# Optimization experiments

Measured on AMD Instinct MI355X. Metric: run time of the kernel, lower is better.

The kernel has to match this reference:

```python
import jax, jax.numpy as jnp
import numpy as np

HEADS = 4
DIM_HEAD = 32
SCALE = DIM_HEAD ** -0.5


def setup_inputs() -> dict:
    key = jax.random.key(0)
    k1, k2, k3 = jax.random.split(key, 3)
    dim = 128
    hidden = HEADS * DIM_HEAD  # 128
    x = jax.random.normal(k1, (4, dim, 64, 64), dtype=jnp.float32)
    w_qkv = jax.random.normal(k2, (3 * hidden, dim), dtype=jnp.float32) * (dim ** -0.5)
    w_out = jax.random.normal(k3, (dim, hidden), dtype=jnp.float32) * (hidden ** -0.5)
    b_out = jnp.zeros((dim,), dtype=jnp.float32)
    return {"x": x, "w_qkv": w_qkv, "w_out": w_out, "b_out": b_out}


def reference(x, w_qkv, w_out, b_out):
    b, c, h, w = x.shape
    n = h * w
    # 1x1 conv == channel matmul per pixel
    qkv = jnp.einsum('oc,bchw->bohw', w_qkv, x)  # [b, 3*hidden, h, w]
    q, k, v = jnp.split(qkv, 3, axis=1)
    # b (heads d) x y -> b heads d (x y)
    def to_heads(t):
        return t.reshape(b, HEADS, DIM_HEAD, n)
    q = to_heads(q) * SCALE
    k = to_heads(k)
    v = to_heads(v)
    sim = jnp.einsum('bhdi,bhdj->bhij', q, k)          # [b, heads, n, n]
    attn = jax.nn.softmax(sim, axis=-1)
    out = jnp.einsum('bhij,bhdj->bhid', attn, v)        # [b, heads, n, d]
    # b h (x y) d -> b (h d) x y
    out = out.transpose(0, 1, 3, 2).reshape(b, HEADS * DIM_HEAD, h, w)
    out = jnp.einsum('oc,bchw->bohw', w_out, out) + b_out[None, :, None, None]
    return out
```

## Files before the change

kernel.cpp:

```cpp
#include <hip/hip_runtime.h>
#include <math.h>

#define NHEAD 4
#define DHEAD 32
#define NPIX  4096
#define CIN   128

typedef __bf16 bf16_t;
typedef __bf16 bf16x8 __attribute__((ext_vector_type(8)));
typedef __bf16 bf16x4 __attribute__((ext_vector_type(4)));
typedef float  f32x4  __attribute__((ext_vector_type(4)));

constexpr float QSCALE = 0.17677669529663687f * 1.4426950408889634f;

__global__ void __launch_bounds__(256) prep_swz(
    const float* __restrict__ wqkv, const float* __restrict__ wout,
    ushort* __restrict__ wq_s, ushort* __restrict__ wo_s) {
  const int gid = blockIdx.x * 256 + threadIdx.x;
  const int lane = gid & 63, n = lane & 15, quad = (lane >> 4) & 3;
  if (gid < 6144) {
    const int ot = gid >> 8, k = (gid >> 6) & 3;
    const float sc = (ot < 8) ? QSCALE : 1.f;
    const float* src = wqkv + (size_t)(ot * 16 + n) * CIN + k * 32 + quad * 8;
    bf16x8 o;
#pragma unroll
    for (int e = 0; e < 8; ++e) o[e] = (bf16_t)(src[e] * sc);
    *(bf16x8*)(wq_s + (size_t)gid * 8) = o;
  } else {
    const int oid = gid - 6144;
    const int ot = oid >> 8, k = (oid >> 6) & 3;
    const float* src = wout + (size_t)(ot * 16 + n) * CIN + k * 32 + quad * 8;
    bf16x8 o;
#pragma unroll
    for (int e = 0; e < 8; ++e) o[e] = (bf16_t)src[e];
    *(bf16x8*)(wo_s + (size_t)oid * 8) = o;
  }
}

__global__ void __launch_bounds__(256) qkv_mfma(
    const float* __restrict__ x, const ushort* __restrict__ wq_s,
    ushort* __restrict__ qb, ushort* __restrict__ kb, ushort* __restrict__ vT) {
  __shared__ ushort Xls[32 * 136];
  const int blk = blockIdx.x, tid = threadIdx.x;
  const int wave = tid >> 6, lane = tid & 63;
  const int n = lane & 15, quad = lane >> 4;
  const int bb = blk >> 7;
  const int p0 = (blk & 127) * 32;

  {
    const int pc = tid & 7, c0 = (tid >> 3) * 4;
    const float* xp = x + ((size_t)bb * CIN + c0) * NPIX + p0 + pc * 4;
    float4 r0 = *(const float4*)xp;
    float4 r1 = *(const float4*)(xp + NPIX);
    float4 r2 = *(const float4*)(xp + 2 * NPIX);
    float4 r3 = *(const float4*)(xp + 3 * NPIX);
    bf16x4 w0 = {(bf16_t)r0.x, (bf16_t)r1.x, (bf16_t)r2.x, (bf16_t)r3.x};
    bf16x4 w1 = {(bf16_t)r0.y, (bf16_t)r1.y, (bf16_t)r2.y, (bf16_t)r3.y};
    bf16x4 w2 = {(bf16_t)r0.z, (bf16_t)r1.z, (bf16_t)r2.z, (bf16_t)r3.z};
    bf16x4 w3 = {(bf16_t)r0.w, (bf16_t)r1.w, (bf16_t)r2.w, (bf16_t)r3.w};
    *(bf16x4*)&Xls[(pc * 4 + 0) * 136 + c0] = w0;
    *(bf16x4*)&Xls[(pc * 4 + 1) * 136 + c0] = w1;
    *(bf16x4*)&Xls[(pc * 4 + 2) * 136 + c0] = w2;
    *(bf16x4*)&Xls[(pc * 4 + 3) * 136 + c0] = w3;
  }
  __syncthreads();

  bf16x8 xf[2][4];
#pragma unroll
  for (int nt = 0; nt < 2; ++nt)
#pragma unroll
    for (int k = 0; k < 4; ++k)
      xf[nt][k] = *(const bf16x8*)&Xls[(nt * 16 + n) * 136 + k * 32 + quad * 8];

#pragma unroll
  for (int mt = 0; mt < 6; ++mt) {
    const int ot = wave * 6 + mt;
    const int type = ot >> 3;
    const int wt = ot & 7, head = wt >> 1, d0 = (wt & 1) * 16;
    const int bh = bb * NHEAD + head;
    bf16x8 wf4[4];
#pragma unroll
    for (int k = 0; k < 4; ++k)
      wf4[k] = *(const bf16x8*)(wq_s + (size_t)((ot * 4 + k) * 64 + lane) * 8);
    f32x4 acc[2] = {{0.f, 0.f, 0.f, 0.f}, {0.f, 0.f, 0.f, 0.f}};
    if (type < 2) {
#pragma unroll
      for (int k = 0; k < 4; ++k)
#pragma unroll
        for (int nt = 0; nt < 2; ++nt)
          acc[nt] = __builtin_amdgcn_mfma_f32_16x16x32_bf16(wf4[k], xf[nt][k], acc[nt], 0, 0, 0);
      ushort* dst = (type == 0) ? qb : kb;
#pragma unroll
      for (int nt = 0; nt < 2; ++nt) {
        bf16x4 o = {(bf16_t)acc[nt][0], (bf16_t)acc[nt][1],
                    (bf16_t)acc[nt][2], (bf16_t)acc[nt][3]};
        *(bf16x4*)(dst + ((size_t)bh * NPIX + p0 + nt * 16 + n) * DHEAD + d0 + quad * 4) = o;
      }
    } else {
#pragma unroll
      for (int k = 0; k < 4; ++k)
#pragma unroll
        for (int nt = 0; nt < 2; ++nt)
          acc[nt] = __builtin_amdgcn_mfma_f32_16x16x32_bf16(xf[nt][k], wf4[k], acc[nt], 0, 0, 0);
#pragma unroll
      for (int nt = 0; nt < 2; ++nt) {
        bf16x4 o = {(bf16_t)acc[nt][0], (bf16_t)acc[nt][1],
                    (bf16_t)acc[nt][2], (bf16_t)acc[nt][3]};
        *(bf16x4*)(vT + ((size_t)bh * DHEAD + d0 + n) * NPIX + p0 + nt * 16 + quad * 4) = o;
      }
    }
  }
}

__device__ __forceinline__ void ft_load(const ushort* kb0, const ushort* vb0,
                                        int t, bf16x8* kf, bf16x8* vf) {
#pragma unroll
  for (int p = 0; p < 2; ++p) {
#pragma unroll
    for (int s = 0; s < 2; ++s)
      kf[p * 2 + s] = *(const bf16x8*)(kb0 + (size_t)(t * 64 + p * 32 + s * 4) * DHEAD);
#pragma unroll
    for (int dp = 0; dp < 2; ++dp)
      vf[p * 2 + dp] = *(const bf16x8*)(vb0 + (size_t)dp * 16 * NPIX + t * 64 + p * 32);
  }
}

__device__ __forceinline__ void ft_compute(const bf16x8* qf, const bf16x8* kf,
                                           const bf16x8* vf, const bf16x8 ones,
                                           f32x4 O[8][2], f32x4* Ol) {
  const f32x4 zero = {0.f, 0.f, 0.f, 0.f};
#pragma unroll
  for (int p = 0; p < 2; ++p) {
#pragma unroll
    for (int rp = 0; rp < 8; ++rp) {
      f32x4 sa = __builtin_amdgcn_mfma_f32_16x16x32_bf16(kf[p * 2 + 0], qf[rp], zero, 0, 0, 0);
      f32x4 sb = __builtin_amdgcn_mfma_f32_16x16x32_bf16(kf[p * 2 + 1], qf[rp], zero, 0, 0, 0);
      bf16x8 pf;
#pragma unroll
      for (int r = 0; r < 4; ++r) {
        pf[r]     = (bf16_t)__builtin_amdgcn_exp2f(sa[r]);
        pf[r + 4] = (bf16_t)__builtin_amdgcn_exp2f(sb[r]);
      }
      O[rp][0] = __builtin_amdgcn_mfma_f32_16x16x32_bf16(pf, vf[p * 2 + 0], O[rp][0], 0, 0, 0);
      O[rp][1] = __builtin_amdgcn_mfma_f32_16x16x32_bf16(pf, vf[p * 2 + 1], O[rp][1], 0, 0, 0);
      Ol[rp]   = __builtin_amdgcn_mfma_f32_16x16x32_bf16(pf, ones, Ol[rp], 0, 0, 0);
    }
  }
}

__global__ void __launch_bounds__(256, 2) flash_mfma(
    const ushort* __restrict__ qb, const ushort* __restrict__ kbuf,
    const ushort* __restrict__ vTb, float* __restrict__ part) {
  const int tid = threadIdx.x, wave = tid >> 6, lane = tid & 63;
  const int n = lane & 15, quad = lane >> 4;
  const int js = blockIdx.y, bh = blockIdx.z;
  const int qrel = blockIdx.x * 512 + wave * 128;

  const ushort* kg = kbuf + (size_t)bh * NPIX * DHEAD;
  const ushort* vg = vTb + (size_t)bh * DHEAD * NPIX;

  bf16x8 qf[8];
#pragma unroll
  for (int rp = 0; rp < 8; ++rp)
    qf[rp] = *(const bf16x8*)(qb +
        ((size_t)bh * NPIX + qrel + rp * 16 + n) * DHEAD + quad * 8);

  f32x4 O[8][2], Ol[8];
#pragma unroll
  for (int rp = 0; rp < 8; ++rp) {
    O[rp][0] = (f32x4){0.f, 0.f, 0.f, 0.f};
    O[rp][1] = (f32x4){0.f, 0.f, 0.f, 0.f};
    Ol[rp]   = (f32x4){0.f, 0.f, 0.f, 0.f};
  }
  const bf16_t one = (bf16_t)1.0f;
  const bf16x8 ones = {one, one, one, one, one, one, one, one};

  const int pk = ((n >> 2) << 3) | (n & 3);
  const ushort* kb0 = kg + (size_t)(js * 1024 + pk) * DHEAD + quad * 8;
  const ushort* vb0 = vg + (size_t)n * NPIX + js * 1024 + quad * 8;

  bf16x8 kA[4], vA[4], kB[4], vB[4];
  ft_load(kb0, vb0, 0, kA, vA);
#pragma unroll 1
  for (int t = 0; t < 16; t += 2) {
    ft_load(kb0, vb0, t + 1, kB, vB);
    ft_compute(qf, kA, vA, ones, O, Ol);
    if (t + 2 < 16) ft_load(kb0, vb0, t + 2, kA, vA);
    ft_compute(qf, kB, vB, ones, O, Ol);
  }

  float* pb = part + ((size_t)js * 65536 + (size_t)bh * NPIX + qrel) * 36;
#pragma unroll
  for (int rp = 0; rp < 8; ++rp)
#pragma unroll
    for (int r = 0; r < 4; ++r) {
      const int q = rp * 16 + quad * 4 + r;
      pb[(size_t)q * 36 + n]      = O[rp][0][r];
      pb[(size_t)q * 36 + 16 + n] = O[rp][1][r];
      if (n == 0) pb[(size_t)q * 36 + 32] = Ol[rp][r];
    }
}

__global__ void __launch_bounds__(256) out_fused(
    const float* __restrict__ part, const ushort* __restrict__ wo_s,
    const float* __restrict__ bias, float* __restrict__ out) {
  const int blk = blockIdx.x, tid = threadIdx.x;
  const int wave = tid >> 6, lane = tid & 63;
  const int n = lane & 15, quad = lane >> 4;
  const int bb = blk >> 7;
  const int p0 = (blk & 127) * 32;
  const int oc0 = wave * 32;

  bf16x8 wf[2][4];
#pragma unroll
  for (int mt = 0; mt < 2; ++mt)
#pragma unroll
    for (int k = 0; k < 4; ++k)
      wf[mt][k] = *(const bf16x8*)(wo_s + (size_t)(((wave * 2 + mt) * 4 + k) * 64 + lane) * 8);

  bf16x8 bfr[2][4];
#pragma unroll
  for (int nt = 0; nt < 2; ++nt) {
    const int px = p0 + nt * 16 + n;
#pragma unroll
    for (int k = 0; k < 4; ++k) {
      const float* pbase = part + ((size_t)(bb * NHEAD + k) * NPIX + px) * 36;
      f32x4 s0 = (f32x4){0.f, 0.f, 0.f, 0.f}, s1 = (f32x4){0.f, 0.f, 0.f, 0.f};
      float l = 0.f;
#pragma unroll
      for (int ks = 0; ks < 4; ++ks) {
        const float* pp = pbase + (size_t)ks * 65536 * 36;
        s0 += *(const f32x4*)(pp + quad * 8);
        s1 += *(const f32x4*)(pp + quad * 8 + 4);
        l += pp[32];
      }
      const float inv = 1.f / l;
      bfr[nt][k] = (bf16x8){(bf16_t)(s0[0] * inv), (bf16_t)(s0[1] * inv),
                            (bf16_t)(s0[2] * inv), (bf16_t)(s0[3] * inv),
                            (bf16_t)(s1[0] * inv), (bf16_t)(s1[1] * inv),
                            (bf16_t)(s1[2] * inv), (bf16_t)(s1[3] * inv)};
    }
  }

  f32x4 acc[2][2];
#pragma unroll
  for (int mt = 0; mt < 2; ++mt)
#pragma unroll
    for (int nt = 0; nt < 2; ++nt) acc[mt][nt] = (f32x4){0.f, 0.f, 0.f, 0.f};
#pragma unroll
  for (int k = 0; k < 4; ++k)
#pragma unroll
    for (int mt = 0; mt < 2; ++mt)
#pragma unroll
      for (int nt = 0; nt < 2; ++nt)
        acc[mt][nt] = __builtin_amdgcn_mfma_f32_16x16x32_bf16(
            wf[mt][k], bfr[nt][k], acc[mt][nt], 0, 0, 0);

#pragma unroll
  for (int mt = 0; mt < 2; ++mt) {
    const int oc = oc0 + mt * 16 + quad * 4;
#pragma unroll
    for (int nt = 0; nt < 2; ++nt)
#pragma unroll
      for (int r = 0; r < 4; ++r)
        out[((size_t)bb * CIN + oc + r) * NPIX + p0 + nt * 16 + n] =
            acc[mt][nt][r] + bias[oc + r];
  }
}

extern "C" void kernel_launch(void* const* d_in, const int* in_sizes, int n_in,
                              void* d_out, int out_size, void* d_ws, size_t ws_size,
                              hipStream_t stream) {
  const float* x     = (const float*)d_in[0];
  const float* w_qkv = (const float*)d_in[1];
  const float* w_out = (const float*)d_in[2];
  const float* b_out = (const float*)d_in[3];
  float* out = (float*)d_out;

  char* base = (char*)d_ws;
  ushort* qb   = (ushort*)base;
  ushort* kb   = (ushort*)(base + (size_t)4 * 1024 * 1024);
  ushort* vT   = (ushort*)(base + (size_t)8 * 1024 * 1024);
  ushort* wq_s = (ushort*)(base + (size_t)12 * 1024 * 1024);
  ushort* wo_s = (ushort*)(base + (size_t)12 * 1024 * 1024 + 256 * 1024);
  float*  part = (float*)(base + (size_t)13 * 1024 * 1024);

  prep_swz<<<dim3(32), 256, 0, stream>>>(w_qkv, w_out, wq_s, wo_s);
  qkv_mfma<<<dim3(512), 256, 0, stream>>>(x, wq_s, qb, kb, vT);
  flash_mfma<<<dim3(8, 4, 16), 256, 0, stream>>>(qb, kb, vT, part);
  out_fused<<<dim3(512), 256, 0, stream>>>(part, wo_s, b_out, out);
}
```

Before: 134.0 us.

## Split KV range eightfold, store bf16 partials, reduce via shared memory

The flash kernel now splits the key range into 8 chunks of 512 instead of 4 chunks of 1024, doubling the grid to 1024 blocks, and raises the launch-bounds occupancy hint from 2 to 4. Partial outputs are stored as bf16 with the row sums in a separate float buffer, which shrinks the partial buffer. The output kernel reduces the 8 partials with coalesced vector loads into LDS before the projection MFMA. The cost is more partial traffic per output pixel, extra bf16 rounding of the unnormalized partial sums, and register pressure under the tighter launch bound.

```diff
diff --git a/kernel.cpp b/kernel.cpp
--- a/kernel.cpp
+++ b/kernel.cpp
@@ -148,9 +148,10 @@
   }
 }
 
-__global__ void __launch_bounds__(256, 2) flash_mfma(
+__global__ void __launch_bounds__(256, 4) flash_mfma(
     const ushort* __restrict__ qb, const ushort* __restrict__ kbuf,
-    const ushort* __restrict__ vTb, float* __restrict__ part) {
+    const ushort* __restrict__ vTb, ushort* __restrict__ pO,
+    float* __restrict__ pl) {
   const int tid = threadIdx.x, wave = tid >> 6, lane = tid & 63;
   const int n = lane & 15, quad = lane >> 4;
   const int js = blockIdx.y, bh = blockIdx.z;
@@ -176,34 +177,37 @@
   const bf16x8 ones = {one, one, one, one, one, one, one, one};
 
   const int pk = ((n >> 2) << 3) | (n & 3);
-  const ushort* kb0 = kg + (size_t)(js * 1024 + pk) * DHEAD + quad * 8;
-  const ushort* vb0 = vg + (size_t)n * NPIX + js * 1024 + quad * 8;
+  const ushort* kb0 = kg + (size_t)(js * 512 + pk) * DHEAD + quad * 8;
+  const ushort* vb0 = vg + (size_t)n * NPIX + js * 512 + quad * 8;
 
   bf16x8 kA[4], vA[4], kB[4], vB[4];
   ft_load(kb0, vb0, 0, kA, vA);
 #pragma unroll 1
-  for (int t = 0; t < 16; t += 2) {
+  for (int t = 0; t < 8; t += 2) {
     ft_load(kb0, vb0, t + 1, kB, vB);
     ft_compute(qf, kA, vA, ones, O, Ol);
-    if (t + 2 < 16) ft_load(kb0, vb0, t + 2, kA, vA);
+    if (t + 2 < 8) ft_load(kb0, vb0, t + 2, kA, vA);
     ft_compute(qf, kB, vB, ones, O, Ol);
   }
 
-  float* pb = part + ((size_t)js * 65536 + (size_t)bh * NPIX + qrel) * 36;
+  ushort* pOb = pO + ((size_t)js * 65536 + (size_t)bh * NPIX + qrel) * 32;
+  float*  plb = pl + (size_t)js * 65536 + (size_t)bh * NPIX + qrel;
 #pragma unroll
   for (int rp = 0; rp < 8; ++rp)
 #pragma unroll
     for (int r = 0; r < 4; ++r) {
       const int q = rp * 16 + quad * 4 + r;
-      pb[(size_t)q * 36 + n]      = O[rp][0][r];
-      pb[(size_t)q * 36 + 16 + n] = O[rp][1][r];
-      if (n == 0) pb[(size_t)q * 36 + 32] = Ol[rp][r];
+      pOb[(size_t)q * 32 + n]      = __builtin_bit_cast(ushort, (bf16_t)O[rp][0][r]);
+      pOb[(size_t)q * 32 + 16 + n] = __builtin_bit_cast(ushort, (bf16_t)O[rp][1][r]);
+      if (n == 0) plb[q] = Ol[rp][r];
     }
 }
 
 __global__ void __launch_bounds__(256) out_fused(
-    const float* __restrict__ part, const ushort* __restrict__ wo_s,
-    const float* __restrict__ bias, float* __restrict__ out) {
+    const ushort* __restrict__ pO, const float* __restrict__ pl,
+    const ushort* __restrict__ wo_s, const float* __restrict__ bias,
+    float* __restrict__ out) {
+  __shared__ ushort AOls[32 * 136];
   const int blk = blockIdx.x, tid = threadIdx.x;
   const int wave = tid >> 6, lane = tid & 63;
   const int n = lane & 15, quad = lane >> 4;
@@ -218,29 +222,45 @@
     for (int k = 0; k < 4; ++k)
       wf[mt][k] = *(const bf16x8*)(wo_s + (size_t)(((wave * 2 + mt) * 4 + k) * 64 + lane) * 8);
 
+  {
+    const int px8 = tid >> 3, c8 = tid & 7;
+    const int h = c8 >> 1, dh = (c8 & 1) * 16;
+    const size_t rowbase = (size_t)(bb * NHEAD + h) * NPIX + p0 + px8;
+    float s[16];
+#pragma unroll
+    for (int e = 0; e < 16; ++e) s[e] = 0.f;
+    float l = 0.f;
+#pragma unroll
+    for (int js = 0; js < 8; ++js) {
+      const ushort* po = pO + ((size_t)js * 65536 + rowbase) * 32 + dh;
+      bf16x8 a = *(const bf16x8*)po;
+      bf16x8 b = *(const bf16x8*)(po + 8);
+#pragma unroll
+      for (int e = 0; e < 8; ++e) {
+        s[e]     += (float)a[e];
+        s[8 + e] += (float)b[e];
+      }
+      l += pl[(size_t)js * 65536 + rowbase];
+    }
+    const float inv = 1.f / l;
+    bf16x8 o0, o1;
+#pragma unroll
+    for (int e = 0; e < 8; ++e) {
+      o0[e] = (bf16_t)(s[e] * inv);
+      o1[e] = (bf16_t)(s[8 + e] * inv);
+    }
+    ushort* dstl = &AOls[px8 * 136 + c8 * 16];
+    *(bf16x8*)dstl = o0;
+    *(bf16x8*)(dstl + 8) = o1;
+  }
+  __syncthreads();
+
   bf16x8 bfr[2][4];
 #pragma unroll
-  for (int nt = 0; nt < 2; ++nt) {
-    const int px = p0 + nt * 16 + n;
-#pragma unroll
-    for (int k = 0; k < 4; ++k) {
-      const float* pbase = part + ((size_t)(bb * NHEAD + k) * NPIX + px) * 36;
-      f32x4 s0 = (f32x4){0.f, 0.f, 0.f, 0.f}, s1 = (f32x4){0.f, 0.f, 0.f, 0.f};
-      float l = 0.f;
-#pragma unroll
-      for (int ks = 0; ks < 4; ++ks) {
-        const float* pp = pbase + (size_t)ks * 65536 * 36;
-        s0 += *(const f32x4*)(pp + quad * 8);
-        s1 += *(const f32x4*)(pp + quad * 8 + 4);
-        l += pp[32];
-      }
-      const float inv = 1.f / l;
-      bfr[nt][k] = (bf16x8){(bf16_t)(s0[0] * inv), (bf16_t)(s0[1] * inv),
-                            (bf16_t)(s0[2] * inv), (bf16_t)(s0[3] * inv),
-                            (bf16_t)(s1[0] * inv), (bf16_t)(s1[1] * inv),
-                            (bf16_t)(s1[2] * inv), (bf16_t)(s1[3] * inv)};
-    }
-  }
+  for (int nt = 0; nt < 2; ++nt)
+#pragma unroll
+    for (int k = 0; k < 4; ++k)
+      bfr[nt][k] = *(const bf16x8*)&AOls[(nt * 16 + n) * 136 + k * 32 + quad * 8];
 
   f32x4 acc[2][2];
 #pragma unroll
@@ -283,10 +303,11 @@
   ushort* vT   = (ushort*)(base + (size_t)8 * 1024 * 1024);
   ushort* wq_s = (ushort*)(base + (size_t)12 * 1024 * 1024);
   ushort* wo_s = (ushort*)(base + (size_t)12 * 1024 * 1024 + 256 * 1024);
-  float*  part = (float*)(base + (size_t)13 * 1024 * 1024);
+  float*  pl   = (float*)(base + (size_t)12 * 1024 * 1024 + 768 * 1024);
+  ushort* pO   = (ushort*)(base + (size_t)15 * 1024 * 1024);
 
   prep_swz<<<dim3(32), 256, 0, stream>>>(w_qkv, w_out, wq_s, wo_s);
   qkv_mfma<<<dim3(512), 256, 0, stream>>>(x, wq_s, qb, kb, vT);
-  flash_mfma<<<dim3(8, 4, 16), 256, 0, stream>>>(qb, kb, vT, part);
-  out_fused<<<dim3(512), 256, 0, stream>>>(part, wo_s, b_out, out);
-}
+  flash_mfma<<<dim3(8, 8, 16), 256, 0, stream>>>(qb, kb, vT, pO, pl);
+  out_fused<<<dim3(512), 256, 0, stream>>>(pO, pl, wo_s, b_out, out);
+}
```

Measured after the change: 411.2 us. 3.07x slower.
